# Optimization experiments

Measured on AMD Instinct MI355X. Metric: run time of the kernel, lower is better.

The kernel has to match this reference:

```python
import jax, jax.numpy as jnp
import numpy as np

B, S, D, H = 8, 1024, 768, 12
DH = D // H  # per-head dim = 64


def setup_inputs() -> dict:
    key = jax.random.key(0)
    ks = jax.random.split(key, 9)
    scale = 1.0 / np.sqrt(D)
    x = jax.random.normal(ks[0], (B, S, D), dtype=jnp.float32)
    # Per-head projection weights stacked over the head axis [H, D, DH]
    Wq = jax.random.normal(ks[1], (H, D, DH), dtype=jnp.float32) * scale
    bq = jax.random.normal(ks[2], (H, DH), dtype=jnp.float32) * 0.02
    Wk = jax.random.normal(ks[3], (H, D, DH), dtype=jnp.float32) * scale
    bk = jax.random.normal(ks[4], (H, DH), dtype=jnp.float32) * 0.02
    Wv = jax.random.normal(ks[5], (H, D, DH), dtype=jnp.float32) * scale
    bv = jax.random.normal(ks[6], (H, DH), dtype=jnp.float32) * 0.02
    Wo = jax.random.normal(ks[7], (D, D), dtype=jnp.float32) * scale
    bo = jax.random.normal(ks[8], (D,), dtype=jnp.float32) * 0.02
    return {"x": x, "Wq": Wq, "bq": bq, "Wk": Wk, "bk": bk,
            "Wv": Wv, "bv": bv, "Wo": Wo, "bo": bo}


def reference(x, Wq, bq, Wk, bk, Wv, bv, Wo, bo):
    # Batched equivalent of the per-head Python loop: each head has its own
    # Q/K/V linear projections (weights stacked on the head axis).
    q = jnp.einsum('bsd,hde->bhse', x, Wq) + bq[None, :, None, :]
    k = jnp.einsum('bsd,hde->bhse', x, Wk) + bk[None, :, None, :]
    v = jnp.einsum('bsd,hde->bhse', x, Wv) + bv[None, :, None, :]
    scores = jnp.einsum('bhse,bhte->bhst', q, k) / jnp.sqrt(jnp.float32(DH))
    attn = jax.nn.softmax(scores, axis=-1)
    out = jnp.einsum('bhst,bhte->bhse', attn, v)  # [B,H,S,DH]
    # concat heads on last dim -> [B,S,H*DH] = [B,S,D]
    out = out.transpose(0, 2, 1, 3).reshape(B, S, D)
    return out @ Wo.T + bo
```

## Files before the change

### kernel.cpp

```cpp
#include <hip/hip_runtime.h>
#include <hip/hip_bf16.h>


typedef unsigned short u16;
typedef unsigned int u32;
typedef __attribute__((ext_vector_type(8))) short bf16x8;
typedef __attribute__((ext_vector_type(8))) unsigned short u16x8;
typedef __attribute__((ext_vector_type(4))) float f32x4;
typedef __attribute__((ext_vector_type(4))) u32 u32x4;

typedef __attribute__((address_space(1))) const u32* gas_u32;
typedef __attribute__((address_space(3))) u32* las_u32;

#define DEVI __device__ __forceinline__

DEVI u16 f2bf(float f) {
  union { float f; u32 u; } v; v.f = f;
  u32 r = v.u + 0x7fffu + ((v.u >> 16) & 1u);
  return (u16)(r >> 16);
}

DEVI void gll16(const void* g, void* l) {
  __builtin_amdgcn_global_load_lds((gas_u32)g, (las_u32)l, 16, 0, 0);
}

DEVI f32x4 mfma16(bf16x8 a, bf16x8 b, f32x4 c) {
  return __builtin_amdgcn_mfma_f32_16x16x32_bf16(a, b, c, 0, 0, 0);
}

DEVI u32 cvtpk(float lo, float hi) {
  u32 r;
  asm("v_cvt_pk_bf16_f32 %0, %1, %2" : "=v"(r) : "v"(lo), "v"(hi));
  return r;
}

__global__ __launch_bounds__(256) void k_prep(const float* __restrict__ x,
                                              u16* __restrict__ xb,
                                              const float* __restrict__ Wo,
                                              u16* __restrict__ Wob,
                                              const float* __restrict__ Wq,
                                              const float* __restrict__ Wk,
                                              const float* __restrict__ Wv,
                                              u16* __restrict__ Wtb) {
  __shared__ u16 T[64][65];
  const int blk = blockIdx.x;
  const int tid = threadIdx.x;
  if (blk < 6720) {
    const float* in; u16* out; int idx;
    if (blk < 6144) { in = x;  out = xb;  idx = blk * 256 + tid; }
    else            { in = Wo; out = Wob; idx = (blk - 6144) * 256 + tid; }
    float4 v = ((const float4*)in)[idx];
    ushort4 o;
    o.x = f2bf(v.x); o.y = f2bf(v.y); o.z = f2bf(v.z); o.w = f2bf(v.w);
    ((ushort4*)out)[idx] = o;
    return;
  }
  const int blk2 = blk - 6720;
  const int th = blk2 / 12;
  const int k0 = (blk2 % 12) * 64;
  const float* W = (th < 12) ? Wq : (th < 24) ? Wk : Wv;
  const int h = th % 12;
  W += (size_t)h * 768 * 64;
  const int row = tid >> 2, c = tid & 3;
  const float* src = W + (size_t)(k0 + row) * 64 + c * 16;
#pragma unroll
  for (int j = 0; j < 4; ++j) {
    float4 v = ((const float4*)src)[j];
    T[row][c * 16 + j * 4 + 0] = f2bf(v.x);
    T[row][c * 16 + j * 4 + 1] = f2bf(v.y);
    T[row][c * 16 + j * 4 + 2] = f2bf(v.z);
    T[row][c * 16 + j * 4 + 3] = f2bf(v.w);
  }
  __syncthreads();
  const int e = tid >> 2;
  u16* dst = Wtb + ((size_t)th * 64 + e) * 768 + k0 + c * 16;
  alignas(16) u16 tmp[16];
#pragma unroll
  for (int j = 0; j < 16; ++j) tmp[j] = T[c * 16 + j][e];
  *(u16x8*)(dst)     = *(const u16x8*)(tmp);
  *(u16x8*)(dst + 8) = *(const u16x8*)(tmp + 8);
}

__global__ __launch_bounds__(256) void k_gemmQKV(const u16* __restrict__ Ab,
                                                 const u16* __restrict__ Wtb,
                                                 const float* __restrict__ bq,
                                                 const float* __restrict__ bk,
                                                 const float* __restrict__ bv,
                                                 u16* __restrict__ Qb,
                                                 u16* __restrict__ VTb) {
  __shared__ u16 smem[2][12288];
  const int tid = threadIdx.x;
  const int w = tid >> 6, lane = tid & 63, lq = lane & 15, g = lane >> 4;
  const int wm = w >> 1, wn = w & 1;
  const int m0 = blockIdx.x * 128;
  const int pn = blockIdx.y;
  const u16* Arows = Ab + (size_t)m0 * 768;
  const u16* Brows = Wtb + (size_t)pn * 64 * 768;

  f32x4 acc[4][2];
#pragma unroll
  for (int mf = 0; mf < 4; ++mf)
#pragma unroll
    for (int nf = 0; nf < 2; ++nf) acc[mf][nf] = (f32x4){0.f, 0.f, 0.f, 0.f};

#define QSTAGE(buf, kt_)                                                         \
  {                                                                              \
    const int kb_ = (kt_) * 64;                                                  \
    _Pragma("unroll")                                                            \
    for (int i = 0; i < 4; ++i) {                                                \
      int c = w * 4 + i;                                                         \
      int id = c * 64 + lane;                                                    \
      int row = id >> 3, cb = id & 7;                                            \
      gll16(Arows + (size_t)row * 768 + kb_ + ((cb ^ (row & 7)) << 3),           \
            &smem[buf][c * 512]);                                                \
    }                                                                            \
    _Pragma("unroll")                                                            \
    for (int i = 0; i < 2; ++i) {                                                \
      int c = w * 2 + i;                                                         \
      int id = c * 64 + lane;                                                    \
      int row = id >> 3, cb = id & 7;                                            \
      gll16(Brows + (size_t)row * 768 + kb_ + ((cb ^ (row & 7)) << 3),           \
            &smem[buf][8192 + c * 512]);                                         \
    }                                                                            \
  }

#define QCOMP(buf)                                                               \
  {                                                                              \
    const u16* As_ = &smem[buf][0];                                              \
    const u16* Bs_ = &smem[buf][8192];                                           \
    _Pragma("unroll")                                                            \
    for (int kk = 0; kk < 2; ++kk) {                                             \
      bf16x8 a[4], b[2];                                                         \
      _Pragma("unroll")                                                          \
      for (int mf = 0; mf < 4; ++mf) {                                           \
        int row = wm * 64 + mf * 16 + lq;                                        \
        a[mf] = *(const bf16x8*)(As_ + row * 64 +                                \
                                 (((kk * 64 + g * 16) ^ ((row & 7) << 4)) >> 1)); \
      }                                                                          \
      _Pragma("unroll")                                                          \
      for (int nf = 0; nf < 2; ++nf) {                                           \
        int row = wn * 32 + nf * 16 + lq;                                        \
        b[nf] = *(const bf16x8*)(Bs_ + row * 64 +                                \
                                 (((kk * 64 + g * 16) ^ ((row & 7) << 4)) >> 1)); \
      }                                                                          \
      _Pragma("unroll")                                                          \
      for (int mf = 0; mf < 4; ++mf)                                             \
        _Pragma("unroll")                                                        \
        for (int nf = 0; nf < 2; ++nf)                                           \
          acc[mf][nf] = mfma16(a[mf], b[nf], acc[mf][nf]);                       \
    }                                                                            \
  }

  QSTAGE(0, 0)
  asm volatile("s_waitcnt vmcnt(0)" ::: "memory");
  __syncthreads();
  for (int it = 0; it < 6; ++it) {
    const int kt = it * 2;
    QSTAGE(1, kt + 1)
    QCOMP(0)
    asm volatile("s_waitcnt vmcnt(0)" ::: "memory");
    __syncthreads();
    if (it < 5) QSTAGE(0, kt + 2)
    QCOMP(1)
    asm volatile("s_waitcnt vmcnt(0)" ::: "memory");
    __syncthreads();
  }
#undef QSTAGE
#undef QCOMP

  const int sel = pn / 12;
  const int ph  = pn % 12;
  const int b = m0 >> 10;
  if (sel == 2) {
    u16* Ct = &smem[0][0];
#pragma unroll
    for (int nf = 0; nf < 2; ++nf) {
      const int e = wn * 32 + nf * 16 + lq;
      const float bi = bv[ph * 64 + e];
#pragma unroll
      for (int mf = 0; mf < 4; ++mf)
#pragma unroll
        for (int r = 0; r < 4; ++r) {
          int sl = wm * 64 + mf * 16 + 4 * g + r;
          Ct[e * 136 + sl] = f2bf(acc[mf][nf][r] + bi);
        }
    }
    __syncthreads();
    const int er = tid >> 2, cc = tid & 3;
    u16* dst = VTb + ((size_t)(b * 12 + ph) * 64 + er) * 1024 + (m0 & 1023) + cc * 32;
#pragma unroll
    for (int i = 0; i < 4; ++i)
      *(u16x8*)(dst + i * 8) = *(const u16x8*)(Ct + er * 136 + cc * 32 + i * 8);
  } else {
    u16* out = Qb + (size_t)sel * 6291456;
    const float qs = sel ? 1.0f : 0.18033688f;
    const float* bp = sel ? bk : bq;
#pragma unroll
    for (int nf = 0; nf < 2; ++nf) {
      const int e = wn * 32 + nf * 16 + lq;
      const float bi = bp[ph * 64 + e];
#pragma unroll
      for (int mf = 0; mf < 4; ++mf)
#pragma unroll
        for (int r = 0; r < 4; ++r) {
          int s = (m0 & 1023) + wm * 64 + mf * 16 + 4 * g + r;
          out[((size_t)(b * 12 + ph) * 1024 + s) * 64 + e] = f2bf((acc[mf][nf][r] + bi) * qs);
        }
    }
  }
}

__global__ __launch_bounds__(256) void k_gemmO(const u16* __restrict__ Ab,
                                               const u16* __restrict__ Bb,
                                               const float* __restrict__ bias,
                                               float* __restrict__ out) {
  __shared__ u16 smem[2][12288];
  const int tid = threadIdx.x;
  const int w = tid >> 6, lane = tid & 63, lq = lane & 15, g = lane >> 4;
  const int wm = w >> 1, wn = w & 1;
  const int m0 = blockIdx.x * 128;
  const int pn = blockIdx.y;
  const u16* Arows = Ab + (size_t)m0 * 768;
  const u16* Brows = Bb + (size_t)pn * 64 * 768;

  f32x4 acc[4][2];
#pragma unroll
  for (int mf = 0; mf < 4; ++mf)
#pragma unroll
    for (int nf = 0; nf < 2; ++nf) acc[mf][nf] = (f32x4){0.f, 0.f, 0.f, 0.f};

#define OSTAGE(buf, kt_)                                                         \
  {                                                                              \
    const int kb_ = (kt_) * 64;                                                  \
    _Pragma("unroll")                                                            \
    for (int i = 0; i < 4; ++i) {                                                \
      int c = w * 4 + i;                                                         \
      int id = c * 64 + lane;                                                    \
      int row = id >> 3, cb = id & 7;                                            \
      gll16(Arows + (size_t)row * 768 + kb_ + ((cb ^ (row & 7)) << 3),           \
            &smem[buf][c * 512]);                                                \
    }                                                                            \
    _Pragma("unroll")                                                            \
    for (int i = 0; i < 2; ++i) {                                                \
      int c = w * 2 + i;                                                         \
      int id = c * 64 + lane;                                                    \
      int row = id >> 3, cb = id & 7;                                            \
      gll16(Brows + (size_t)row * 768 + kb_ + ((cb ^ (row & 7)) << 3),           \
            &smem[buf][8192 + c * 512]);                                         \
    }                                                                            \
  }

#define OCOMP(buf)                                                               \
  {                                                                              \
    const u16* As_ = &smem[buf][0];                                              \
    const u16* Bs_ = &smem[buf][8192];                                           \
    _Pragma("unroll")                                                            \
    for (int kk = 0; kk < 2; ++kk) {                                             \
      bf16x8 a[4], b[2];                                                         \
      _Pragma("unroll")                                                          \
      for (int mf = 0; mf < 4; ++mf) {                                           \
        int row = wm * 64 + mf * 16 + lq;                                        \
        a[mf] = *(const bf16x8*)(As_ + row * 64 +                                \
                                 (((kk * 64 + g * 16) ^ ((row & 7) << 4)) >> 1)); \
      }                                                                          \
      _Pragma("unroll")                                                          \
      for (int nf = 0; nf < 2; ++nf) {                                           \
        int row = wn * 32 + nf * 16 + lq;                                        \
        b[nf] = *(const bf16x8*)(Bs_ + row * 64 +                                \
                                 (((kk * 64 + g * 16) ^ ((row & 7) << 4)) >> 1)); \
      }                                                                          \
      _Pragma("unroll")                                                          \
      for (int mf = 0; mf < 4; ++mf)                                             \
        _Pragma("unroll")                                                        \
        for (int nf = 0; nf < 2; ++nf)                                           \
          acc[mf][nf] = mfma16(a[mf], b[nf], acc[mf][nf]);                       \
    }                                                                            \
  }

  OSTAGE(0, 0)
  asm volatile("s_waitcnt vmcnt(0)" ::: "memory");
  __syncthreads();
  for (int it = 0; it < 6; ++it) {
    const int kt = it * 2;
    OSTAGE(1, kt + 1)
    OCOMP(0)
    asm volatile("s_waitcnt vmcnt(0)" ::: "memory");
    __syncthreads();
    if (it < 5) OSTAGE(0, kt + 2)
    OCOMP(1)
    asm volatile("s_waitcnt vmcnt(0)" ::: "memory");
    __syncthreads();
  }
#undef OSTAGE
#undef OCOMP

#pragma unroll
  for (int nf = 0; nf < 2; ++nf) {
    const int n = pn * 64 + wn * 32 + nf * 16 + lq;
    const float bi = bias[n];
#pragma unroll
    for (int mf = 0; mf < 4; ++mf)
#pragma unroll
      for (int r = 0; r < 4; ++r) {
        int m = m0 + wm * 64 + mf * 16 + 4 * g + r;
        out[(size_t)m * 768 + n] = acc[mf][nf][r] + bi;
      }
  }
}

__global__ __launch_bounds__(512) void k_attn(const u16* __restrict__ Qb,
                                              const u16* __restrict__ Kb,
                                              const u16* __restrict__ VTb,
                                              u16* __restrict__ AO) {
  __shared__ u16 Ksm[2][4096];
  __shared__ u16 Vsm[2][4096];
  const int tid = threadIdx.x;
  const int w = tid >> 6, lane = tid & 63, lq = lane & 15, g = lane >> 4;
  const int bh = blockIdx.x, b = bh / 12, h = bh % 12;
  const int q0 = blockIdx.y * 128 + w * 16;
  const u16* Qw = Qb + ((size_t)bh * 1024 + q0) * 64;
  const u16* Kp = Kb + (size_t)bh * 65536;
  const u16* Vp = VTb + (size_t)bh * 65536;
  const bool gsel = (g & 1);

  bf16x8 qf[2];
#pragma unroll
  for (int kk = 0; kk < 2; ++kk)
    qf[kk] = *(const bf16x8*)(Qw + lq * 64 + kk * 32 + g * 8);

  f32x4 o[4];
#pragma unroll
  for (int ef = 0; ef < 4; ++ef) o[ef] = (f32x4){0.f, 0.f, 0.f, 0.f};
  float l_ = 0.f;

#define STAGE(buf, kt_)                                                          \
  {                                                                              \
    const int kb_ = (kt_) * 64;                                                  \
    const int id = w * 64 + lane;                                                \
    const int row = id >> 3, cb = id & 7;                                        \
    const int sb = cb ^ (row & 7);                                               \
    const int tb = (sb & 4) | ((sb & 1) << 1) | ((sb >> 1) & 1);                 \
    gll16(Kp + (size_t)(kb_ + row) * 64 + (sb << 3), &Ksm[buf][w * 512]);        \
    gll16(Vp + (size_t)row * 1024 + kb_ + (tb << 3), &Vsm[buf][w * 512]);        \
  }

#define TILE(buf)                                                                \
  {                                                                              \
    f32x4 s[4];                                                                  \
    _Pragma("unroll")                                                            \
    for (int kf = 0; kf < 4; ++kf) s[kf] = (f32x4){0.f, 0.f, 0.f, 0.f};          \
    __builtin_amdgcn_s_setprio(1);                                               \
    _Pragma("unroll")                                                            \
    for (int kf = 0; kf < 4; ++kf) {                                             \
      const int row = kf * 16 + lq;                                              \
      _Pragma("unroll")                                                          \
      for (int kk = 0; kk < 2; ++kk) {                                           \
        bf16x8 kfr = *(const bf16x8*)(&Ksm[buf][0] + row * 64 +                  \
                                      (((kk * 64 + g * 16) ^ ((row & 7) << 4)) >> 1)); \
        s[kf] = mfma16(kfr, qf[kk], s[kf]);                                      \
      }                                                                          \
    }                                                                            \
    __builtin_amdgcn_s_setprio(0);                                               \
    float sm = 0.f;                                                              \
    _Pragma("unroll")                                                            \
    for (int kf = 0; kf < 4; ++kf)                                               \
      _Pragma("unroll")                                                          \
      for (int r = 0; r < 4; ++r) {                                              \
        float p = __builtin_amdgcn_exp2f(s[kf][r]);                              \
        s[kf][r] = p;                                                            \
        sm += p;                                                                 \
      }                                                                          \
    l_ += sm;                                                                    \
    u32 D[4][2];                                                                 \
    _Pragma("unroll")                                                            \
    for (int kf = 0; kf < 4; ++kf) {                                             \
      D[kf][0] = cvtpk(s[kf][0], s[kf][1]);                                      \
      D[kf][1] = cvtpk(s[kf][2], s[kf][3]);                                      \
    }                                                                            \
    _Pragma("unroll")                                                            \
    for (int kk = 0; kk < 2; ++kk) {                                             \
      const int kk2 = kk * 2;                                                    \
      u32 sa0 = gsel ? D[kk2][0] : D[kk2 + 1][0];                                \
      u32 sa1 = gsel ? D[kk2][1] : D[kk2 + 1][1];                                \
      u32 xa0 = __shfl_xor(sa0, 16), xa1 = __shfl_xor(sa1, 16);                  \
      u32x4 t = { gsel ? xa0 : D[kk2][0],                                        \
                  gsel ? xa1 : D[kk2][1],                                        \
                  gsel ? D[kk2 + 1][0] : xa0,                                    \
                  gsel ? D[kk2 + 1][1] : xa1 };                                  \
      bf16x8 pb = __builtin_bit_cast(bf16x8, t);                                 \
      __builtin_amdgcn_s_setprio(1);                                             \
      _Pragma("unroll")                                                          \
      for (int ef = 0; ef < 4; ++ef) {                                           \
        const int row = ef * 16 + lq;                                            \
        bf16x8 vf = *(const bf16x8*)(&Vsm[buf][0] + row * 64 +                   \
                                     (((kk * 64 + g * 16) ^ ((row & 7) << 4)) >> 1)); \
        o[ef] = mfma16(vf, pb, o[ef]);                                           \
      }                                                                          \
      __builtin_amdgcn_s_setprio(0);                                             \
    }                                                                            \
  }

  STAGE(0, 0)
  asm volatile("s_waitcnt vmcnt(0)" ::: "memory");
  __syncthreads();

  for (int it = 0; it < 8; ++it) {
    const int kt = it * 2;
    STAGE(1, kt + 1)
    TILE(0)
    asm volatile("s_waitcnt vmcnt(0)" ::: "memory");
    __syncthreads();
    if (it < 7) STAGE(0, kt + 2)
    TILE(1)
    asm volatile("s_waitcnt vmcnt(0)" ::: "memory");
    __syncthreads();
  }

  l_ += __shfl_xor(l_, 16);
  l_ += __shfl_xor(l_, 32);

  const float inv = 1.0f / l_;
  u16* dst = AO + ((size_t)(b * 1024 + q0 + lq)) * 768 + h * 64 + g * 4;
#pragma unroll
  for (int ef = 0; ef < 4; ++ef) {
    ushort4 t;
    t.x = f2bf(o[ef][0] * inv);
    t.y = f2bf(o[ef][1] * inv);
    t.z = f2bf(o[ef][2] * inv);
    t.w = f2bf(o[ef][3] * inv);
    *(ushort4*)(dst + ef * 16) = t;
  }
#undef STAGE
#undef TILE
}

extern "C" void kernel_launch(void* const* d_in, const int* in_sizes, int n_in,
                              void* d_out, int out_size, void* d_ws, size_t ws_size,
                              hipStream_t stream) {
  (void)in_sizes; (void)n_in; (void)out_size; (void)ws_size;
  const float* x  = (const float*)d_in[0];
  const float* Wq = (const float*)d_in[1];
  const float* bq = (const float*)d_in[2];
  const float* Wk = (const float*)d_in[3];
  const float* bk = (const float*)d_in[4];
  const float* Wv = (const float*)d_in[5];
  const float* bv = (const float*)d_in[6];
  const float* Wo = (const float*)d_in[7];
  const float* bo = (const float*)d_in[8];

  char* ws = (char*)d_ws;
  u16* xb  = (u16*)(ws);
  u16* Wtb = (u16*)(ws + 12582912);
  u16* Wob = (u16*)(ws + 12582912 + 3538944);
  u16* Qb  = (u16*)(ws + 12582912 + 3538944 + 1179648);
  u16* Kb  = Qb + (size_t)96 * 1024 * 64;
  u16* VTb = Kb + (size_t)96 * 1024 * 64;
  u16* AO  = xb;

  k_prep<<<7152, 256, 0, stream>>>(x, xb, Wo, Wob, Wq, Wk, Wv, Wtb);

  k_gemmQKV<<<dim3(64, 36), 256, 0, stream>>>(xb, Wtb, bq, bk, bv, Qb, VTb);

  k_attn<<<dim3(96, 8), 512, 0, stream>>>(Qb, Kb, VTb, AO);

  k_gemmO<<<dim3(64, 12), 256, 0, stream>>>(AO, Wob, bo, (float*)d_out);
}
```

Baseline: 106.8 us.

## Load K/V fragments directly from global in attention, drop LDS staging

The attention kernel no longer stages K and V tiles through double-buffered shared memory with barriers. Each wave now loads its MFMA operand fragments straight from global memory, relying on L1/L2 for reuse across waves. Blocks shrink from 512 to 256 threads, covering 64 query rows each, so the grid doubles. This removes LDS traffic and __syncthreads stalls, but every wave issues redundant global loads of the same K/V data and no longer prefetches the next tile.

```diff
diff --git a/kernel.cpp b/kernel.cpp
--- a/kernel.cpp
+++ b/kernel.cpp
@@ -308,20 +308,19 @@
   }
 }
 
-__global__ __launch_bounds__(512) void k_attn(const u16* __restrict__ Qb,
-                                              const u16* __restrict__ Kb,
-                                              const u16* __restrict__ VTb,
-                                              u16* __restrict__ AO) {
-  __shared__ u16 Ksm[2][4096];
-  __shared__ u16 Vsm[2][4096];
+__global__ __launch_bounds__(256, 4) void k_attn(const u16* __restrict__ Qb,
+                                                 const u16* __restrict__ Kb,
+                                                 const u16* __restrict__ VTb,
+                                                 u16* __restrict__ AO) {
   const int tid = threadIdx.x;
   const int w = tid >> 6, lane = tid & 63, lq = lane & 15, g = lane >> 4;
   const int bh = blockIdx.x, b = bh / 12, h = bh % 12;
-  const int q0 = blockIdx.y * 128 + w * 16;
+  const int q0 = blockIdx.y * 64 + w * 16;
   const u16* Qw = Qb + ((size_t)bh * 1024 + q0) * 64;
   const u16* Kp = Kb + (size_t)bh * 65536;
   const u16* Vp = VTb + (size_t)bh * 65536;
   const bool gsel = (g & 1);
+  const int vchunk = ((g & 1) << 1) + (g >> 1);
 
   bf16x8 qf[2];
 #pragma unroll
@@ -333,87 +332,72 @@
   for (int ef = 0; ef < 4; ++ef) o[ef] = (f32x4){0.f, 0.f, 0.f, 0.f};
   float l_ = 0.f;
 
-#define STAGE(buf, kt_)                                                          \
-  {                                                                              \
-    const int kb_ = (kt_) * 64;                                                  \
-    const int id = w * 64 + lane;                                                \
-    const int row = id >> 3, cb = id & 7;                                        \
-    const int sb = cb ^ (row & 7);                                               \
-    const int tb = (sb & 4) | ((sb & 1) << 1) | ((sb >> 1) & 1);                 \
-    gll16(Kp + (size_t)(kb_ + row) * 64 + (sb << 3), &Ksm[buf][w * 512]);        \
-    gll16(Vp + (size_t)row * 1024 + kb_ + (tb << 3), &Vsm[buf][w * 512]);        \
-  }
-
-#define TILE(buf)                                                                \
-  {                                                                              \
-    f32x4 s[4];                                                                  \
-    _Pragma("unroll")                                                            \
-    for (int kf = 0; kf < 4; ++kf) s[kf] = (f32x4){0.f, 0.f, 0.f, 0.f};          \
-    __builtin_amdgcn_s_setprio(1);                                               \
-    _Pragma("unroll")                                                            \
-    for (int kf = 0; kf < 4; ++kf) {                                             \
-      const int row = kf * 16 + lq;                                              \
-      _Pragma("unroll")                                                          \
-      for (int kk = 0; kk < 2; ++kk) {                                           \
-        bf16x8 kfr = *(const bf16x8*)(&Ksm[buf][0] + row * 64 +                  \
-                                      (((kk * 64 + g * 16) ^ ((row & 7) << 4)) >> 1)); \
-        s[kf] = mfma16(kfr, qf[kk], s[kf]);                                      \
-      }                                                                          \
-    }                                                                            \
-    __builtin_amdgcn_s_setprio(0);                                               \
-    float sm = 0.f;                                                              \
-    _Pragma("unroll")                                                            \
-    for (int kf = 0; kf < 4; ++kf)                                               \
-      _Pragma("unroll")                                                          \
-      for (int r = 0; r < 4; ++r) {                                              \
-        float p = __builtin_amdgcn_exp2f(s[kf][r]);                              \
-        s[kf][r] = p;                                                            \
-        sm += p;                                                                 \
-      }                                                                          \
-    l_ += sm;                                                                    \
-    u32 D[4][2];                                                                 \
-    _Pragma("unroll")                                                            \
-    for (int kf = 0; kf < 4; ++kf) {                                             \
-      D[kf][0] = cvtpk(s[kf][0], s[kf][1]);                                      \
-      D[kf][1] = cvtpk(s[kf][2], s[kf][3]);                                      \
-    }                                                                            \
-    _Pragma("unroll")                                                            \
-    for (int kk = 0; kk < 2; ++kk) {                                             \
-      const int kk2 = kk * 2;                                                    \
-      u32 sa0 = gsel ? D[kk2][0] : D[kk2 + 1][0];                                \
-      u32 sa1 = gsel ? D[kk2][1] : D[kk2 + 1][1];                                \
-      u32 xa0 = __shfl_xor(sa0, 16), xa1 = __shfl_xor(sa1, 16);                  \
-      u32x4 t = { gsel ? xa0 : D[kk2][0],                                        \
-                  gsel ? xa1 : D[kk2][1],                                        \
-                  gsel ? D[kk2 + 1][0] : xa0,                                    \
-                  gsel ? D[kk2 + 1][1] : xa1 };                                  \
-      bf16x8 pb = __builtin_bit_cast(bf16x8, t);                                 \
-      __builtin_amdgcn_s_setprio(1);                                             \
-      _Pragma("unroll")                                                          \
-      for (int ef = 0; ef < 4; ++ef) {                                           \
-        const int row = ef * 16 + lq;                                            \
-        bf16x8 vf = *(const bf16x8*)(&Vsm[buf][0] + row * 64 +                   \
-                                     (((kk * 64 + g * 16) ^ ((row & 7) << 4)) >> 1)); \
-        o[ef] = mfma16(vf, pb, o[ef]);                                           \
-      }                                                                          \
-      __builtin_amdgcn_s_setprio(0);                                             \
-    }                                                                            \
-  }
-
-  STAGE(0, 0)
-  asm volatile("s_waitcnt vmcnt(0)" ::: "memory");
-  __syncthreads();
-
-  for (int it = 0; it < 8; ++it) {
-    const int kt = it * 2;
-    STAGE(1, kt + 1)
-    TILE(0)
-    asm volatile("s_waitcnt vmcnt(0)" ::: "memory");
-    __syncthreads();
-    if (it < 7) STAGE(0, kt + 2)
-    TILE(1)
-    asm volatile("s_waitcnt vmcnt(0)" ::: "memory");
-    __syncthreads();
+  const u16* Krow = Kp + (size_t)lq * 64 + g * 8;
+  const u16* Vrow = Vp + (size_t)lq * 1024 + vchunk * 8;
+
+  for (int kt = 0; kt < 16; ++kt) {
+    const int kb = kt * 64;
+
+    bf16x8 kfr[4][2];
+#pragma unroll
+    for (int kf = 0; kf < 4; ++kf)
+#pragma unroll
+      for (int kk = 0; kk < 2; ++kk)
+        kfr[kf][kk] = *(const bf16x8*)(Krow + (size_t)(kb + kf * 16) * 64 + kk * 32);
+
+    f32x4 s[4];
+#pragma unroll
+    for (int kf = 0; kf < 4; ++kf) s[kf] = (f32x4){0.f, 0.f, 0.f, 0.f};
+    __builtin_amdgcn_s_setprio(1);
+#pragma unroll
+    for (int kf = 0; kf < 4; ++kf)
+#pragma unroll
+      for (int kk = 0; kk < 2; ++kk)
+        s[kf] = mfma16(kfr[kf][kk], qf[kk], s[kf]);
+    __builtin_amdgcn_s_setprio(0);
+
+    bf16x8 vf[4][2];
+#pragma unroll
+    for (int ef = 0; ef < 4; ++ef)
+#pragma unroll
+      for (int kk = 0; kk < 2; ++kk)
+        vf[ef][kk] = *(const bf16x8*)(Vrow + (size_t)(ef * 16) * 1024 + kb + kk * 32);
+
+    float sm = 0.f;
+#pragma unroll
+    for (int kf = 0; kf < 4; ++kf)
+#pragma unroll
+      for (int r = 0; r < 4; ++r) {
+        float p = __builtin_amdgcn_exp2f(s[kf][r]);
+        s[kf][r] = p;
+        sm += p;
+      }
+    l_ += sm;
+
+    u32 D[4][2];
+#pragma unroll
+    for (int kf = 0; kf < 4; ++kf) {
+      D[kf][0] = cvtpk(s[kf][0], s[kf][1]);
+      D[kf][1] = cvtpk(s[kf][2], s[kf][3]);
+    }
+
+#pragma unroll
+    for (int kk = 0; kk < 2; ++kk) {
+      const int kk2 = kk * 2;
+      u32 sa0 = gsel ? D[kk2][0] : D[kk2 + 1][0];
+      u32 sa1 = gsel ? D[kk2][1] : D[kk2 + 1][1];
+      u32 xa0 = __shfl_xor(sa0, 16), xa1 = __shfl_xor(sa1, 16);
+      u32x4 t = { gsel ? xa0 : D[kk2][0],
+                  gsel ? xa1 : D[kk2][1],
+                  gsel ? D[kk2 + 1][0] : xa0,
+                  gsel ? D[kk2 + 1][1] : xa1 };
+      bf16x8 pb = __builtin_bit_cast(bf16x8, t);
+      __builtin_amdgcn_s_setprio(1);
+#pragma unroll
+      for (int ef = 0; ef < 4; ++ef)
+        o[ef] = mfma16(vf[ef][kk], pb, o[ef]);
+      __builtin_amdgcn_s_setprio(0);
+    }
   }
 
   l_ += __shfl_xor(l_, 16);
@@ -430,8 +414,6 @@
     t.w = f2bf(o[ef][3] * inv);
     *(ushort4*)(dst + ef * 16) = t;
   }
-#undef STAGE
-#undef TILE
 }
 
 extern "C" void kernel_launch(void* const* d_in, const int* in_sizes, int n_in,
@@ -461,7 +443,7 @@
 
   k_gemmQKV<<<dim3(64, 36), 256, 0, stream>>>(xb, Wtb, bq, bk, bv, Qb, VTb);
 
-  k_attn<<<dim3(96, 8), 512, 0, stream>>>(Qb, Kb, VTb, AO);
+  k_attn<<<dim3(96, 16), 256, 0, stream>>>(Qb, Kb, VTb, AO);
 
   k_gemmO<<<dim3(64, 12), 256, 0, stream>>>(AO, Wob, bo, (float*)d_out);
 }
```

After: 264.1 us. 147% more time.
